# Performance work log

Hardware: AMD Instinct MI355X
Metric: run time of the kernel (lower is better)

The kernel has to match this reference:

```python
import jax, jax.numpy as jnp
import numpy as np

N = 10000
E = 160000
IN_C = 512
OUT_C = 1024
NEG_SLOPE = 0.2


def setup_inputs() -> dict:
    key = jax.random.key(0)
    ks = jax.random.split(key, 12)
    x = jax.random.normal(ks[0], (N, IN_C), dtype=jnp.float32)
    edge_index = jax.random.randint(ks[1], (2, E), 0, N, dtype=jnp.int32)
    s_in = 1.0 / np.sqrt(IN_C)
    s_out = 1.0 / np.sqrt(OUT_C)
    return {
        "x": x,
        "edge_index": edge_index,
        "W1": jax.random.normal(ks[2], (IN_C, OUT_C), dtype=jnp.float32) * s_in,
        "a_src1": jax.random.normal(ks[3], (OUT_C,), dtype=jnp.float32) * s_out,
        "a_dst1": jax.random.normal(ks[4], (OUT_C,), dtype=jnp.float32) * s_out,
        "b1": jnp.zeros((OUT_C,), dtype=jnp.float32),
        "W2": jax.random.normal(ks[5], (IN_C, OUT_C), dtype=jnp.float32) * s_in,
        "a_src2": jax.random.normal(ks[6], (OUT_C,), dtype=jnp.float32) * s_out,
        "a_dst2": jax.random.normal(ks[7], (OUT_C,), dtype=jnp.float32) * s_out,
        "b2": jnp.zeros((OUT_C,), dtype=jnp.float32),
        "prelu_a": jnp.asarray(0.25, dtype=jnp.float32),
        "Wp1": jax.random.normal(ks[8], (OUT_C, OUT_C), dtype=jnp.float32) * s_out,
        "bp1": jnp.zeros((OUT_C,), dtype=jnp.float32),
        "Wp2": jax.random.normal(ks[9], (OUT_C, 1024), dtype=jnp.float32) * s_out,
    }


def _gat_conv(x, src, dst, W, a_src, a_dst, b):
    # x: [N, in], W: [in, out]. PyG GATConv, heads=1, self-loops already in src/dst.
    h = x @ W  # [N, out]
    alpha_s = h @ a_src  # [N]
    alpha_d = h @ a_dst  # [N]
    e = alpha_s[src] + alpha_d[dst]  # [E+N]
    e = jnp.where(e >= 0, e, NEG_SLOPE * e)  # LeakyReLU(0.2)
    # segment softmax over destination nodes
    m = jax.ops.segment_max(e, dst, num_segments=N)  # [N]
    ex = jnp.exp(e - m[dst])
    denom = jax.ops.segment_sum(ex, dst, num_segments=N)  # [N], >=1 via self-loops
    alpha = ex / denom[dst]  # [E+N]
    out = jax.ops.segment_sum(alpha[:, None] * h[src], dst, num_segments=N)
    return out + b


def reference(x, edge_index, W1, a_src1, a_dst1, b1, W2, a_src2, a_dst2, b2,
              prelu_a, Wp1, bp1, Wp2):
    # add self loops (PyG GATConv default)
    loops = jnp.arange(N, dtype=edge_index.dtype)
    src = jnp.concatenate([edge_index[0], loops])
    dst = jnp.concatenate([edge_index[1], loops])

    def prelu(v):
        return jnp.where(v >= 0, v, prelu_a * v)

    h1 = prelu(_gat_conv(x, src, dst, W1, a_src1, a_dst1, b1))  # [N, 1024]
    h2 = prelu(_gat_conv(x, src, dst, W2, a_src2, a_dst2, b2))  # [N, 1024]
    h = h1 + h2

    # semantic attention: project -> mean over nodes -> softmax over 1024 dims
    w = jnp.tanh(h @ Wp1 + bp1) @ Wp2  # [N, 1024]
    w = w.mean(axis=0)  # [1024]
    att = jax.nn.softmax(w, axis=0)  # [1024] == beta.mean(0).squeeze()
    return att * h1 + (1.0 - att) * h2
```

## Files before the change

### kernel.cpp

```cpp
#include <hip/hip_runtime.h>

#define IN_C 512
#define OUT_C 1024
#define NC2 2048
#define NEG_SLOPE 0.2f

typedef short frag8 __attribute__((ext_vector_type(8)));
typedef float f32x4 __attribute__((ext_vector_type(4)));
typedef int i32x4 __attribute__((ext_vector_type(4)));

#define GLOAD_LDS16(g, l) __builtin_amdgcn_global_load_lds(\
    (const __attribute__((address_space(1))) void*)(g), \
    (__attribute__((address_space(3))) void*)(l), 16, 0, 0)

__device__ __forceinline__ unsigned short f2b(float f){
  unsigned u = __float_as_uint(f);
  unsigned r = (u + 0x7fffu + ((u >> 16) & 1u)) >> 16;
  return (unsigned short)r;
}
__device__ __forceinline__ unsigned encf(float f){
  unsigned u = __float_as_uint(f);
  return (u & 0x80000000u) ? ~u : (u | 0x80000000u);
}
__device__ __forceinline__ float decf(unsigned u){
  unsigned v = (u & 0x80000000u) ? (u & 0x7fffffffu) : ~u;
  return __uint_as_float(v);
}
__device__ __forceinline__ float leaky(float v){ return v >= 0.f ? v : NEG_SLOPE * v; }


__global__ void prep_kernel(const float* __restrict__ W1, const float* __restrict__ W2,
                            const float* __restrict__ Wp1,
                            const float* __restrict__ a_src1, const float* __restrict__ a_dst1,
                            const float* __restrict__ a_src2, const float* __restrict__ a_dst2,
                            unsigned short* __restrict__ WT, unsigned short* __restrict__ Wp1T,
                            float* __restrict__ uv){
  __shared__ float tile[32][33];
  int b = blockIdx.x;
  int tx = threadIdx.x & 31, ty = threadIdx.x >> 5;
  if (b < 1024){
    const float* in = (b >> 9) ? W2 : W1;
    int rowOff = (b >> 9) * OUT_C;
    int bb = b & 511;
    int c0 = (bb & 31) * 32, r0 = (bb >> 5) * 32;
    for (int i = ty; i < 32; i += 8)
      tile[i][tx] = in[(size_t)(r0 + i) * OUT_C + c0 + tx];
    __syncthreads();
    for (int i = ty; i < 32; i += 8)
      WT[(size_t)(c0 + i + rowOff) * IN_C + r0 + tx] = f2b(tile[tx][i]);
  } else if (b < 2048){
    int bb = b - 1024;
    int c0 = (bb & 31) * 32, r0 = (bb >> 5) * 32;
    for (int i = ty; i < 32; i += 8)
      tile[i][tx] = Wp1[(size_t)(r0 + i) * OUT_C + c0 + tx];
    __syncthreads();
    for (int i = ty; i < 32; i += 8)
      Wp1T[(size_t)(c0 + i) * OUT_C + r0 + tx] = f2b(tile[tx][i]);
  } else {
    int g = (b - 2048) * 4 + (threadIdx.x >> 6);
    int lane = threadIdx.x & 63;
    int which = g >> 9;
    int i = g & 511;
    const float* W = (which < 2) ? W1 : W2;
    const float* a = (which == 0) ? a_src1 : (which == 1) ? a_dst1 : (which == 2) ? a_src2 : a_dst2;
    const float* row = W + (size_t)i * OUT_C;
    float s = 0.f;
    for (int j = lane; j < OUT_C; j += 64) s += row[j] * a[j];
    for (int off = 32; off; off >>= 1) s += __shfl_down(s, off);
    if (lane == 0) uv[which * IN_C + i] = s;
  }
}


__global__ void alpha_kernel(const float* __restrict__ x, const float* __restrict__ uv,
                             unsigned short* __restrict__ xb,
                             float* __restrict__ as1, float* __restrict__ ad1,
                             float* __restrict__ as2, float* __restrict__ ad2,
                             float* __restrict__ self1, float* __restrict__ self2,
                             unsigned* __restrict__ m1e, unsigned* __restrict__ m2e,
                             int* counts, int* cursor, float* colsum, float* wv){
  int n = blockIdx.x;
  int w = threadIdx.x >> 6, lane = threadIdx.x & 63;
  __shared__ float sh[4];
  if (threadIdx.x == 0){ counts[n] = 0; cursor[n] = 0; }
  if (n < 8){
    int i = n * 256 + threadIdx.x;
    if (i < 1024) colsum[i] = 0.f; else wv[i - 1024] = 0.f;
  }
  const float* row = x + (size_t)n * IN_C;
  const float* u = uv + w * IN_C;
  float s = 0.f;
  for (int j = lane; j < IN_C; j += 64){
    float v = row[j];
    s += v * u[j];
    if (w == 0) xb[(size_t)n * IN_C + j] = f2b(v);
  }
  for (int off = 32; off; off >>= 1) s += __shfl_down(s, off);
  if (lane == 0){
    sh[w] = s;
    if (w == 0) as1[n] = s;
    else if (w == 1) ad1[n] = s;
    else if (w == 2) as2[n] = s;
    else ad2[n] = s;
  }
  __syncthreads();
  if (threadIdx.x == 0){
    float e1 = leaky(sh[0] + sh[1]);
    float e2 = leaky(sh[2] + sh[3]);
    self1[n] = e1; self2[n] = e2;
    m1e[n] = encf(e1); m2e[n] = encf(e2);
  }
}


__global__ void histmax_kernel(const int* __restrict__ src, const int* __restrict__ dst,
                               const float* __restrict__ as1, const float* __restrict__ ad1,
                               const float* __restrict__ as2, const float* __restrict__ ad2,
                               int* counts, unsigned* m1e, unsigned* m2e, int E){
  int e = blockIdx.x * 256 + threadIdx.x;
  if (e >= E) return;
  int s = src[e], d = dst[e];
  atomicAdd(&counts[d], 1);
  atomicMax(&m1e[d], encf(leaky(as1[s] + ad1[d])));
  atomicMax(&m2e[d], encf(leaky(as2[s] + ad2[d])));
}

__global__ void scanA_kernel(const int* __restrict__ counts, int* __restrict__ offs,
                             int* __restrict__ bsum, int n){
  __shared__ int wsum[4];
  int i = blockIdx.x * 256 + threadIdx.x;
  int wave = threadIdx.x >> 6, lane = threadIdx.x & 63;
  int v = (i < n) ? counts[i] : 0;
  int sc = v;
  for (int o = 1; o < 64; o <<= 1){
    int t = __shfl_up(sc, o);
    if (lane >= o) sc += t;
  }
  if (lane == 63) wsum[wave] = sc;
  __syncthreads();
  int wp = 0, tot = 0;
#pragma unroll
  for (int k = 0; k < 4; k++){
    int ws = wsum[k];
    if (k < wave) wp += ws;
    tot += ws;
  }
  if (i < n) offs[i] = wp + sc - v;
  if (threadIdx.x == 0) bsum[blockIdx.x] = tot;
}

__global__ void scanB_kernel(int* __restrict__ bsum, int nb){
  int lane = threadIdx.x;
  int v = (lane < nb) ? bsum[lane] : 0;
  int sc = v;
  for (int o = 1; o < 64; o <<= 1){
    int t = __shfl_up(sc, o);
    if (lane >= o) sc += t;
  }
  if (lane < nb) bsum[lane] = sc - v;
}

__global__ void scanC_kernel(int* __restrict__ offs, const int* __restrict__ bsum, int n){
  int i = blockIdx.x * 256 + threadIdx.x;
  if (i < n) offs[i] += bsum[blockIdx.x];
}

__global__ void denominit_kernel(const unsigned* __restrict__ m1e, const unsigned* __restrict__ m2e,
                                 const float* __restrict__ self1, const float* __restrict__ self2,
                                 float* __restrict__ m1, float* __restrict__ m2,
                                 float* __restrict__ den1, float* __restrict__ den2, int N){
  int i = blockIdx.x * 256 + threadIdx.x;
  if (i >= N) return;
  float a = decf(m1e[i]), b = decf(m2e[i]);
  m1[i] = a; m2[i] = b;
  den1[i] = expf(self1[i] - a);
  den2[i] = expf(self2[i] - b);
}

__global__ void scatterexp_kernel(const int* __restrict__ src, const int* __restrict__ dst,
                                  const int* __restrict__ offs, int* cursor,
                                  const float* __restrict__ as1, const float* __restrict__ ad1,
                                  const float* __restrict__ as2, const float* __restrict__ ad2,
                                  const float* __restrict__ m1, const float* __restrict__ m2,
                                  int* __restrict__ nsrc, float* __restrict__ nw1, float* __restrict__ nw2,
                                  float* den1, float* den2, int E){
  int e = blockIdx.x * 256 + threadIdx.x;
  if (e >= E) return;
  int s = src[e], d = dst[e];
  int p = atomicAdd(&cursor[d], 1);
  int idx = offs[d] + p;
  float x1 = expf(leaky(as1[s] + ad1[d]) - m1[d]);
  float x2 = expf(leaky(as2[s] + ad2[d]) - m2[d]);
  nsrc[idx] = s; nw1[idx] = x1; nw2[idx] = x2;
  atomicAdd(&den1[d], x1);
  atomicAdd(&den2[d], x2);
}


#define AGG_FMA8(ACC, W, U) \
  ACC[0] += (W) * __uint_as_float(((unsigned)(U).x) << 16); \
  ACC[1] += (W) * __uint_as_float(((unsigned)(U).x) & 0xffff0000u); \
  ACC[2] += (W) * __uint_as_float(((unsigned)(U).y) << 16); \
  ACC[3] += (W) * __uint_as_float(((unsigned)(U).y) & 0xffff0000u); \
  ACC[4] += (W) * __uint_as_float(((unsigned)(U).z) << 16); \
  ACC[5] += (W) * __uint_as_float(((unsigned)(U).z) & 0xffff0000u); \
  ACC[6] += (W) * __uint_as_float(((unsigned)(U).w) << 16); \
  ACC[7] += (W) * __uint_as_float(((unsigned)(U).w) & 0xffff0000u);

__global__ __launch_bounds__(256) void aggx_kernel(
    const int* __restrict__ counts, const int* __restrict__ offs,
    const int* __restrict__ nsrc, const float* __restrict__ nw1, const float* __restrict__ nw2,
    const float* __restrict__ den1, const float* __restrict__ den2,
    const float* __restrict__ self1, const float* __restrict__ self2,
    const float* __restrict__ m1, const float* __restrict__ m2,
    const unsigned short* __restrict__ xb,
    unsigned short* __restrict__ xa1b, unsigned short* __restrict__ xa2b, int N){
  int tid = threadIdx.x;
  int g = tid >> 4, hl = tid & 15;
  int grpbase = tid & 48;
  int d = blockIdx.y * 16 + g;
  if (d >= N) return;
  int colbase = blockIdx.x * 128 + hl * 8;
  float inv1 = 1.f / den1[d], inv2 = 1.f / den2[d];
  int deg = counts[d], off = offs[d];
  float acc1[8] = {0,0,0,0,0,0,0,0}, acc2[8] = {0,0,0,0,0,0,0,0};
  const unsigned short* Xb = xb + colbase;
  for (int base = 0; base < deg; base += 16){
    int i = base + hl;
    int s = 0; float w1 = 0.f, w2 = 0.f;
    if (i < deg){
      int p = off + i;
      s = nsrc[p];
      w1 = nw1[p] * inv1;
      w2 = nw2[p] * inv2;
    }
    int cnt = min(16, deg - base);
#pragma unroll 4
    for (int j = 0; j < cnt; j++){
      int sj = __shfl(s, grpbase + j);
      float w1j = __shfl(w1, grpbase + j);
      float w2j = __shfl(w2, grpbase + j);
      int4 u = *(const int4*)(Xb + (size_t)sj * IN_C);
      AGG_FMA8(acc1, w1j, u)
      AGG_FMA8(acc2, w2j, u)
    }
  }
  {
    float ws1 = expf(self1[d] - m1[d]) * inv1;
    float ws2 = expf(self2[d] - m2[d]) * inv2;
    int4 u = *(const int4*)(Xb + (size_t)d * IN_C);
    AGG_FMA8(acc1, ws1, u)
    AGG_FMA8(acc2, ws2, u)
  }
  size_t outb = (size_t)d * IN_C + colbase;
  i32x4 o1, o2;
  o1.x = (int)((unsigned)f2b(acc1[0]) | ((unsigned)f2b(acc1[1]) << 16));
  o1.y = (int)((unsigned)f2b(acc1[2]) | ((unsigned)f2b(acc1[3]) << 16));
  o1.z = (int)((unsigned)f2b(acc1[4]) | ((unsigned)f2b(acc1[5]) << 16));
  o1.w = (int)((unsigned)f2b(acc1[6]) | ((unsigned)f2b(acc1[7]) << 16));
  o2.x = (int)((unsigned)f2b(acc2[0]) | ((unsigned)f2b(acc2[1]) << 16));
  o2.y = (int)((unsigned)f2b(acc2[2]) | ((unsigned)f2b(acc2[3]) << 16));
  o2.z = (int)((unsigned)f2b(acc2[4]) | ((unsigned)f2b(acc2[5]) << 16));
  o2.w = (int)((unsigned)f2b(acc2[6]) | ((unsigned)f2b(acc2[7]) << 16));
  __builtin_nontemporal_store(o1, (i32x4*)(xa1b + outb));
  __builtin_nontemporal_store(o2, (i32x4*)(xa2b + outb));
}


__global__ __launch_bounds__(256, 2) void gemmh_kernel(const unsigned short* __restrict__ A1,
                                                       const unsigned short* __restrict__ A2,
                                                       const unsigned short* __restrict__ BT,
                                                       const float* __restrict__ b1,
                                                       const float* __restrict__ b2,
                                                       const float* __restrict__ prelu_a,
                                                       unsigned short* __restrict__ hsum,
                                                       unsigned short* __restrict__ hdiff,
                                                       int M, int Mtiles, int perx){
  const int bid = blockIdx.x;
  const int xcd = bid & 7;
  const int li = bid >> 3;
  const int bn_t = li & 7;
  const int bm_t = xcd * perx + (li >> 3);
  if (bm_t >= Mtiles) return;
  const int bm = bm_t * 128, bn = bn_t * 128;
  __shared__ unsigned short Al[2][128 * 32];
  __shared__ unsigned short Bl[2][128 * 32];
  const int t = threadIdx.x;
  const int lane = t & 63, wid = t >> 6;
  const int wr = wid >> 1, wc = wid & 1;
  const int l16 = lane & 15, q = lane >> 4;
  const int qs = (q ^ ((l16 >> 1) & 3)) * 8;
  const int lch = (((lane & 3) ^ ((lane >> 3) & 3)) * 8);
  f32x4 acc1[4][4] = {};
  f32x4 acc2[4][4] = {};
  const int srow = wid * 32 + (lane >> 2);
  const int ga0 = min(bm + srow, M - 1);
  const int ga1 = min(bm + srow + 16, M - 1);
  const unsigned short* pa1_0 = A1 + (size_t)ga0 * IN_C + lch;
  const unsigned short* pa1_1 = A1 + (size_t)ga1 * IN_C + lch;
  const unsigned short* pa2_0 = A2 + (size_t)ga0 * IN_C + lch;
  const unsigned short* pa2_1 = A2 + (size_t)ga1 * IN_C + lch;
  const unsigned short* pb1_0 = BT + (size_t)(bn + srow) * IN_C + lch;
  const unsigned short* pb1_1 = BT + (size_t)(bn + srow + 16) * IN_C + lch;
  const unsigned short* pb2_0 = pb1_0 + (size_t)OUT_C * IN_C;
  const unsigned short* pb2_1 = pb1_1 + (size_t)OUT_C * IN_C;
  const int so0 = (wid * 32) * 32;
  const int so1 = (wid * 32 + 16) * 32;

  for (int k0 = 0; k0 < IN_C; k0 += 32){
    GLOAD_LDS16(pa1_0 + k0, &Al[0][so0]);
    GLOAD_LDS16(pa1_1 + k0, &Al[0][so1]);
    GLOAD_LDS16(pa2_0 + k0, &Al[1][so0]);
    GLOAD_LDS16(pa2_1 + k0, &Al[1][so1]);
    GLOAD_LDS16(pb1_0 + k0, &Bl[0][so0]);
    GLOAD_LDS16(pb1_1 + k0, &Bl[0][so1]);
    GLOAD_LDS16(pb2_0 + k0, &Bl[1][so0]);
    GLOAD_LDS16(pb2_1 + k0, &Bl[1][so1]);
    __syncthreads();
    {
      frag8 af[4], bf[4];
#pragma unroll
      for (int mi = 0; mi < 4; mi++) af[mi] = *(const frag8*)&Al[0][(wr*64 + mi*16 + l16) * 32 + qs];
#pragma unroll
      for (int nj = 0; nj < 4; nj++) bf[nj] = *(const frag8*)&Bl[0][(wc*64 + nj*16 + l16) * 32 + qs];
#pragma unroll
      for (int mi = 0; mi < 4; mi++)
#pragma unroll
        for (int nj = 0; nj < 4; nj++)
          acc1[mi][nj] = __builtin_amdgcn_mfma_f32_16x16x32_bf16(af[mi], bf[nj], acc1[mi][nj], 0, 0, 0);
    }
    {
      frag8 af[4], bf[4];
#pragma unroll
      for (int mi = 0; mi < 4; mi++) af[mi] = *(const frag8*)&Al[1][(wr*64 + mi*16 + l16) * 32 + qs];
#pragma unroll
      for (int nj = 0; nj < 4; nj++) bf[nj] = *(const frag8*)&Bl[1][(wc*64 + nj*16 + l16) * 32 + qs];
#pragma unroll
      for (int mi = 0; mi < 4; mi++)
#pragma unroll
        for (int nj = 0; nj < 4; nj++)
          acc2[mi][nj] = __builtin_amdgcn_mfma_f32_16x16x32_bf16(af[mi], bf[nj], acc2[mi][nj], 0, 0, 0);
    }
    __syncthreads();
  }

  float pa = prelu_a[0];
#pragma unroll
  for (int mi = 0; mi < 4; mi++){
#pragma unroll
    for (int r = 0; r < 4; r++){
      int row = bm + wr*64 + mi*16 + q*4 + r;
      if (row >= M) continue;
#pragma unroll
      for (int nj = 0; nj < 4; nj++){
        int col = bn + wc*64 + nj*16 + l16;
        float v1 = acc1[mi][nj][r] + b1[col];
        v1 = v1 >= 0.f ? v1 : pa * v1;
        float v2 = acc2[mi][nj][r] + b2[col];
        v2 = v2 >= 0.f ? v2 : pa * v2;
        size_t idx = (size_t)row * OUT_C + col;
        __builtin_nontemporal_store(f2b(v1 + v2), &hsum[idx]);
        __builtin_nontemporal_store(f2b(v1 - v2), &hdiff[idx]);
      }
    }
  }
}


__global__ __launch_bounds__(256, 2) void gemm2_kernel(const unsigned short* __restrict__ A,
                                                       const unsigned short* __restrict__ BT,
                                                       const float* __restrict__ bp1,
                                                       float* __restrict__ colsum,
                                                       int M, int Mtiles, int perx){
  const int bid = blockIdx.x;
  const int xcd = bid & 7;
  const int li = bid >> 3;
  const int bn_t = li & 7;
  const int bm_t = xcd * perx + (li >> 3);
  if (bm_t >= Mtiles) return;
  const int bm = bm_t * 128, bn = bn_t * 128;
  __shared__ unsigned short Al[128 * 32];
  __shared__ unsigned short Bl[128 * 32];
  __shared__ float cs[128];
  const int t = threadIdx.x;
  const int lane = t & 63, wid = t >> 6;
  const int wr = wid >> 1, wc = wid & 1;
  const int l16 = lane & 15, q = lane >> 4;
  const int qs = (q ^ ((l16 >> 1) & 3)) * 8;
  const int lch = (((lane & 3) ^ ((lane >> 3) & 3)) * 8);
  if (t < 128) cs[t] = 0.f;
  f32x4 acc[4][4] = {};
  const int srow = wid * 32 + (lane >> 2);
  const int ga0 = min(bm + srow, M - 1);
  const int ga1 = min(bm + srow + 16, M - 1);
  const unsigned short* pa_0 = A + (size_t)ga0 * OUT_C + lch;
  const unsigned short* pa_1 = A + (size_t)ga1 * OUT_C + lch;
  const unsigned short* pb_0 = BT + (size_t)(bn + srow) * OUT_C + lch;
  const unsigned short* pb_1 = BT + (size_t)(bn + srow + 16) * OUT_C + lch;
  const int so0 = (wid * 32) * 32;
  const int so1 = (wid * 32 + 16) * 32;

  for (int k0 = 0; k0 < OUT_C; k0 += 32){
    GLOAD_LDS16(pa_0 + k0, &Al[so0]);
    GLOAD_LDS16(pa_1 + k0, &Al[so1]);
    GLOAD_LDS16(pb_0 + k0, &Bl[so0]);
    GLOAD_LDS16(pb_1 + k0, &Bl[so1]);
    __syncthreads();
    frag8 af[4], bf[4];
#pragma unroll
    for (int mi = 0; mi < 4; mi++) af[mi] = *(const frag8*)&Al[(wr*64 + mi*16 + l16) * 32 + qs];
#pragma unroll
    for (int nj = 0; nj < 4; nj++) bf[nj] = *(const frag8*)&Bl[(wc*64 + nj*16 + l16) * 32 + qs];
#pragma unroll
    for (int mi = 0; mi < 4; mi++)
#pragma unroll
      for (int nj = 0; nj < 4; nj++)
        acc[mi][nj] = __builtin_amdgcn_mfma_f32_16x16x32_bf16(af[mi], bf[nj], acc[mi][nj], 0, 0, 0);
    __syncthreads();
  }

#pragma unroll
  for (int nj = 0; nj < 4; nj++){
    int col = bn + wc*64 + nj*16 + l16;
    float bias = bp1[col];
    float p = 0.f;
#pragma unroll
    for (int mi = 0; mi < 4; mi++){
#pragma unroll
      for (int r = 0; r < 4; r++){
        int row = bm + wr*64 + mi*16 + q*4 + r;
        float tv = tanhf(acc[mi][nj][r] + bias);
        if (row < M) p += tv;
      }
    }
    p += __shfl_xor(p, 16);
    p += __shfl_xor(p, 32);
    if (q == 0) atomicAdd(&cs[wc*64 + nj*16 + l16], p);
  }
  __syncthreads();
  if (t < 128) atomicAdd(&colsum[bn + t], cs[t]);
}


__global__ void wproj_kernel(const float* __restrict__ colsum, const float* __restrict__ Wp2,
                             float* __restrict__ wv){
  int o = blockIdx.x * 256 + threadIdx.x;
  int c0 = blockIdx.y * 128;
  float acc = 0.f;
  for (int c = c0; c < c0 + 128; c++) acc += colsum[c] * Wp2[(size_t)c * OUT_C + o];
  atomicAdd(&wv[o], acc);
}

__global__ __launch_bounds__(1024) void softmax_kernel(const float* __restrict__ wv,
                                                       float* __restrict__ att, float invN){
  int o = threadIdx.x;
  __shared__ float red[1024];
  float w = wv[o] * invN;
  red[o] = w; __syncthreads();
  for (int s = 512; s > 0; s >>= 1){ if (o < s) red[o] = fmaxf(red[o], red[o + s]); __syncthreads(); }
  float m = red[0]; __syncthreads();
  float e = expf(w - m);
  red[o] = e; __syncthreads();
  for (int s = 512; s > 0; s >>= 1){ if (o < s) red[o] += red[o + s]; __syncthreads(); }
  att[o] = e / red[0];
}

__global__ void combine_kernel(const float* __restrict__ att, const unsigned short* __restrict__ hs,
                               const unsigned short* __restrict__ hd, float* __restrict__ out, int total8){
  int i = blockIdx.x * 256 + threadIdx.x;
  if (i >= total8) return;
  int colb = (i & 127) * 8;
  int4 us = ((const int4*)hs)[i];
  int4 ud = ((const int4*)hd)[i];
  float4 a0 = *(const float4*)(att + colb);
  float4 a1 = *(const float4*)(att + colb + 4);
  float o[8]; float sv, dv;
  sv = __uint_as_float(((unsigned)us.x) << 16);        dv = __uint_as_float(((unsigned)ud.x) << 16);
  o[0] = 0.5f * sv + (a0.x - 0.5f) * dv;
  sv = __uint_as_float(((unsigned)us.x) & 0xffff0000u); dv = __uint_as_float(((unsigned)ud.x) & 0xffff0000u);
  o[1] = 0.5f * sv + (a0.y - 0.5f) * dv;
  sv = __uint_as_float(((unsigned)us.y) << 16);        dv = __uint_as_float(((unsigned)ud.y) << 16);
  o[2] = 0.5f * sv + (a0.z - 0.5f) * dv;
  sv = __uint_as_float(((unsigned)us.y) & 0xffff0000u); dv = __uint_as_float(((unsigned)ud.y) & 0xffff0000u);
  o[3] = 0.5f * sv + (a0.w - 0.5f) * dv;
  sv = __uint_as_float(((unsigned)us.z) << 16);        dv = __uint_as_float(((unsigned)ud.z) << 16);
  o[4] = 0.5f * sv + (a1.x - 0.5f) * dv;
  sv = __uint_as_float(((unsigned)us.z) & 0xffff0000u); dv = __uint_as_float(((unsigned)ud.z) & 0xffff0000u);
  o[5] = 0.5f * sv + (a1.y - 0.5f) * dv;
  sv = __uint_as_float(((unsigned)us.w) << 16);        dv = __uint_as_float(((unsigned)ud.w) << 16);
  o[6] = 0.5f * sv + (a1.z - 0.5f) * dv;
  sv = __uint_as_float(((unsigned)us.w) & 0xffff0000u); dv = __uint_as_float(((unsigned)ud.w) & 0xffff0000u);
  o[7] = 0.5f * sv + (a1.w - 0.5f) * dv;
  f32x4 f0; f0[0] = o[0]; f0[1] = o[1]; f0[2] = o[2]; f0[3] = o[3];
  f32x4 f1; f1[0] = o[4]; f1[1] = o[5]; f1[2] = o[6]; f1[3] = o[7];
  __builtin_nontemporal_store(f0, (f32x4*)(out + (size_t)i * 8));
  __builtin_nontemporal_store(f1, (f32x4*)(out + (size_t)i * 8 + 4));
}


extern "C" void kernel_launch(void* const* d_in, const int* in_sizes, int n_in,
                              void* d_out, int out_size, void* d_ws, size_t ws_size,
                              hipStream_t stream){
  const float* x      = (const float*)d_in[0];
  const int*   edge   = (const int*)d_in[1];
  const float* W1     = (const float*)d_in[2];
  const float* a_src1 = (const float*)d_in[3];
  const float* a_dst1 = (const float*)d_in[4];
  const float* b1     = (const float*)d_in[5];
  const float* W2     = (const float*)d_in[6];
  const float* a_src2 = (const float*)d_in[7];
  const float* a_dst2 = (const float*)d_in[8];
  const float* b2     = (const float*)d_in[9];
  const float* prelu_a= (const float*)d_in[10];
  const float* Wp1    = (const float*)d_in[11];
  const float* bp1    = (const float*)d_in[12];
  const float* Wp2    = (const float*)d_in[13];
  const int N = in_sizes[0] / IN_C;
  const int E = in_sizes[1] / 2;
  const int* srcArr = edge;
  const int* dstArr = edge + E;

  char* ws = (char*)d_ws;
  size_t o = 0;
  auto alloc = [&](size_t b) -> char* {
    char* p = ws + o;
    o = (o + b + 255) & ~(size_t)255;
    return p;
  };
  unsigned short* xb    = (unsigned short*)alloc((size_t)N * IN_C * 2);
  unsigned short* WT    = (unsigned short*)alloc((size_t)NC2 * IN_C * 2);
  unsigned short* Wp1T  = (unsigned short*)alloc((size_t)OUT_C * OUT_C * 2);
  unsigned short* xa1b  = (unsigned short*)alloc((size_t)N * IN_C * 2);
  unsigned short* xa2b  = (unsigned short*)alloc((size_t)N * IN_C * 2);
  unsigned short* hsum  = (unsigned short*)alloc((size_t)N * OUT_C * 2);
  unsigned short* hdiff = (unsigned short*)alloc((size_t)N * OUT_C * 2);
  float*          uv    = (float*)alloc(4 * IN_C * 4);
  float*          as1   = (float*)alloc((size_t)4 * N * 4);
  float* ad1 = as1 + N; float* as2 = as1 + 2 * N; float* ad2 = as1 + 3 * N;
  float*          self1 = (float*)alloc((size_t)2 * N * 4); float* self2 = self1 + N;
  unsigned*       m1e   = (unsigned*)alloc((size_t)2 * N * 4); unsigned* m2e = m1e + N;
  float*          m1    = (float*)alloc((size_t)2 * N * 4); float* m2 = m1 + N;
  float*          den1  = (float*)alloc((size_t)2 * N * 4); float* den2 = den1 + N;
  int*            counts= (int*)alloc((size_t)N * 4);
  int*            offs  = (int*)alloc((size_t)(N + 1) * 4);
  int*            cursor= (int*)alloc((size_t)N * 4);
  int*            bsum  = (int*)alloc(64 * 4);
  int*            nsrc  = (int*)alloc((size_t)E * 4);
  float*          nw1   = (float*)alloc((size_t)E * 4);
  float*          nw2   = (float*)alloc((size_t)E * 4);
  float*          colsum= (float*)alloc(OUT_C * 4);
  float*          wv    = (float*)alloc(OUT_C * 4);
  float*          att   = (float*)alloc(OUT_C * 4);

  const int Mtiles = (N + 127) / 128;
  const int perx = (Mtiles + 7) / 8;
  const int gemmgrid = 8 * perx * 8;
  const int nchunk = (N + 255) / 256;

  prep_kernel<<<2560, 256, 0, stream>>>(W1, W2, Wp1, a_src1, a_dst1, a_src2, a_dst2, WT, Wp1T, uv);
  alpha_kernel<<<N, 256, 0, stream>>>(x, uv, xb, as1, ad1, as2, ad2, self1, self2, m1e, m2e,
                                      counts, cursor, colsum, wv);
  histmax_kernel<<<(E + 255) / 256, 256, 0, stream>>>(srcArr, dstArr, as1, ad1, as2, ad2,
                                                      counts, m1e, m2e, E);
  scanA_kernel<<<nchunk, 256, 0, stream>>>(counts, offs, bsum, N);
  scanB_kernel<<<1, 64, 0, stream>>>(bsum, nchunk);
  scanC_kernel<<<nchunk, 256, 0, stream>>>(offs, bsum, N);
  denominit_kernel<<<nchunk, 256, 0, stream>>>(m1e, m2e, self1, self2, m1, m2, den1, den2, N);
  scatterexp_kernel<<<(E + 255) / 256, 256, 0, stream>>>(srcArr, dstArr, offs, cursor,
                                                         as1, ad1, as2, ad2, m1, m2,
                                                         nsrc, nw1, nw2, den1, den2, E);
  aggx_kernel<<<dim3(4, (N + 15) / 16), 256, 0, stream>>>(counts, offs, nsrc, nw1, nw2, den1, den2,
                                                          self1, self2, m1, m2, xb, xa1b, xa2b, N);
  gemmh_kernel<<<gemmgrid, 256, 0, stream>>>(xa1b, xa2b, WT, b1, b2, prelu_a,
                                             hsum, hdiff, N, Mtiles, perx);
  gemm2_kernel<<<gemmgrid, 256, 0, stream>>>(hsum, Wp1T, bp1, colsum, N, Mtiles, perx);
  wproj_kernel<<<dim3(4, 8), 256, 0, stream>>>(colsum, Wp2, wv);
  softmax_kernel<<<1, 1024, 0, stream>>>(wv, att, 1.0f / (float)N);
  combine_kernel<<<(N * OUT_C / 8 + 255) / 256, 256, 0, stream>>>(att, hsum, hdiff, (float*)d_out,
                                                                  N * OUT_C / 8);
}
```

Baseline: 339.3 us.

## Use 256x256 triple-buffered GEMM tiles and store h1/h2 instead of sum/diff

Both GEMMs move from 128x128 tiles with 256 threads to 256x256 tiles with 512 threads and a three-stage LDS pipeline that waits with explicit vmcnt counts, so each step needs one barrier instead of two. gemmh now computes h1 and h2 in separate blocks and stores them directly. gemm2 forms h1+h2 on the fly by loading both through registers and adding them in bf16 before writing to LDS. The aim is more data reuse per block and better overlap of loads with MFMA work. The cost is heavier register and LDS pressure, an extra global read stream in gemm2, and a different tile-to-XCD mapping.

```diff
diff --git a/kernel.cpp b/kernel.cpp
--- a/kernel.cpp
+++ b/kernel.cpp
@@ -27,6 +27,13 @@
   return __uint_as_float(v);
 }
 __device__ __forceinline__ float leaky(float v){ return v >= 0.f ? v : NEG_SLOPE * v; }
+__device__ __forceinline__ int badd(int a, int b){
+  float a0 = __uint_as_float(((unsigned)a) << 16);
+  float a1 = __uint_as_float(((unsigned)a) & 0xffff0000u);
+  float b0 = __uint_as_float(((unsigned)b) << 16);
+  float b1 = __uint_as_float(((unsigned)b) & 0xffff0000u);
+  return (int)((unsigned)f2b(a0 + b0) | ((unsigned)f2b(a1 + b1) << 16));
+}
 
 
 __global__ void prep_kernel(const float* __restrict__ W1, const float* __restrict__ W2,
@@ -267,157 +274,178 @@
 }
 
 
-__global__ __launch_bounds__(256, 2) void gemmh_kernel(const unsigned short* __restrict__ A1,
+#define COMP256(AB, BB) do{ \
+    frag8 af[8], bf[4]; \
+    _Pragma("unroll") \
+    for (int mi = 0; mi < 8; mi++) af[mi] = *(const frag8*)&(AB)[(wr*128 + mi*16 + l16) * 32 + qs]; \
+    _Pragma("unroll") \
+    for (int nj = 0; nj < 4; nj++) bf[nj] = *(const frag8*)&(BB)[(wc*64 + nj*16 + l16) * 32 + qs]; \
+    _Pragma("unroll") \
+    for (int mi = 0; mi < 8; mi++) \
+      _Pragma("unroll") \
+      for (int nj = 0; nj < 4; nj++) \
+        acc[mi][nj] = __builtin_amdgcn_mfma_f32_16x16x32_bf16(af[mi], bf[nj], acc[mi][nj], 0, 0, 0); \
+  }while(0)
+
+
+__global__ __launch_bounds__(512, 2) void gemmh_kernel(const unsigned short* __restrict__ A1,
                                                        const unsigned short* __restrict__ A2,
                                                        const unsigned short* __restrict__ BT,
                                                        const float* __restrict__ b1,
                                                        const float* __restrict__ b2,
                                                        const float* __restrict__ prelu_a,
-                                                       unsigned short* __restrict__ hsum,
-                                                       unsigned short* __restrict__ hdiff,
-                                                       int M, int Mtiles, int perx){
-  const int bid = blockIdx.x;
-  const int xcd = bid & 7;
-  const int li = bid >> 3;
-  const int bn_t = li & 7;
-  const int bm_t = xcd * perx + (li >> 3);
-  if (bm_t >= Mtiles) return;
-  const int bm = bm_t * 128, bn = bn_t * 128;
-  __shared__ unsigned short Al[2][128 * 32];
-  __shared__ unsigned short Bl[2][128 * 32];
+                                                       unsigned short* __restrict__ h1,
+                                                       unsigned short* __restrict__ h2,
+                                                       int M, int Mtiles){
+  const int per = Mtiles;
+  const int sw = (blockIdx.x & 7) * per + (blockIdx.x >> 3);
+  const int bm = (sw >> 3) * 256;
+  const int g  = (sw >> 2) & 1;
+  const int bn = (sw & 3) * 256;
+  __shared__ unsigned short Al[3][256 * 32];
+  __shared__ unsigned short Bl[3][256 * 32];
   const int t = threadIdx.x;
   const int lane = t & 63, wid = t >> 6;
-  const int wr = wid >> 1, wc = wid & 1;
+  const int wr = wid >> 2, wc = wid & 3;
   const int l16 = lane & 15, q = lane >> 4;
   const int qs = (q ^ ((l16 >> 1) & 3)) * 8;
   const int lch = (((lane & 3) ^ ((lane >> 3) & 3)) * 8);
-  f32x4 acc1[4][4] = {};
-  f32x4 acc2[4][4] = {};
-  const int srow = wid * 32 + (lane >> 2);
-  const int ga0 = min(bm + srow, M - 1);
-  const int ga1 = min(bm + srow + 16, M - 1);
-  const unsigned short* pa1_0 = A1 + (size_t)ga0 * IN_C + lch;
-  const unsigned short* pa1_1 = A1 + (size_t)ga1 * IN_C + lch;
-  const unsigned short* pa2_0 = A2 + (size_t)ga0 * IN_C + lch;
-  const unsigned short* pa2_1 = A2 + (size_t)ga1 * IN_C + lch;
-  const unsigned short* pb1_0 = BT + (size_t)(bn + srow) * IN_C + lch;
-  const unsigned short* pb1_1 = BT + (size_t)(bn + srow + 16) * IN_C + lch;
-  const unsigned short* pb2_0 = pb1_0 + (size_t)OUT_C * IN_C;
-  const unsigned short* pb2_1 = pb1_1 + (size_t)OUT_C * IN_C;
-  const int so0 = (wid * 32) * 32;
-  const int so1 = (wid * 32 + 16) * 32;
-
-  for (int k0 = 0; k0 < IN_C; k0 += 32){
-    GLOAD_LDS16(pa1_0 + k0, &Al[0][so0]);
-    GLOAD_LDS16(pa1_1 + k0, &Al[0][so1]);
-    GLOAD_LDS16(pa2_0 + k0, &Al[1][so0]);
-    GLOAD_LDS16(pa2_1 + k0, &Al[1][so1]);
-    GLOAD_LDS16(pb1_0 + k0, &Bl[0][so0]);
-    GLOAD_LDS16(pb1_1 + k0, &Bl[0][so1]);
-    GLOAD_LDS16(pb2_0 + k0, &Bl[1][so0]);
-    GLOAD_LDS16(pb2_1 + k0, &Bl[1][so1]);
-    __syncthreads();
-    {
-      frag8 af[4], bf[4];
-#pragma unroll
-      for (int mi = 0; mi < 4; mi++) af[mi] = *(const frag8*)&Al[0][(wr*64 + mi*16 + l16) * 32 + qs];
-#pragma unroll
-      for (int nj = 0; nj < 4; nj++) bf[nj] = *(const frag8*)&Bl[0][(wc*64 + nj*16 + l16) * 32 + qs];
-#pragma unroll
-      for (int mi = 0; mi < 4; mi++)
-#pragma unroll
-        for (int nj = 0; nj < 4; nj++)
-          acc1[mi][nj] = __builtin_amdgcn_mfma_f32_16x16x32_bf16(af[mi], bf[nj], acc1[mi][nj], 0, 0, 0);
-    }
-    {
-      frag8 af[4], bf[4];
-#pragma unroll
-      for (int mi = 0; mi < 4; mi++) af[mi] = *(const frag8*)&Al[1][(wr*64 + mi*16 + l16) * 32 + qs];
-#pragma unroll
-      for (int nj = 0; nj < 4; nj++) bf[nj] = *(const frag8*)&Bl[1][(wc*64 + nj*16 + l16) * 32 + qs];
-#pragma unroll
-      for (int mi = 0; mi < 4; mi++)
-#pragma unroll
-        for (int nj = 0; nj < 4; nj++)
-          acc2[mi][nj] = __builtin_amdgcn_mfma_f32_16x16x32_bf16(af[mi], bf[nj], acc2[mi][nj], 0, 0, 0);
-    }
-    __syncthreads();
-  }
-
+  f32x4 acc[8][4] = {};
+  const unsigned short* Asrc = g ? A2 : A1;
+  const int r0 = wid * 16 + (lane >> 2);
+  const unsigned short* pa0 = Asrc + (size_t)min(bm + r0,       M - 1) * IN_C + lch;
+  const unsigned short* pa1 = Asrc + (size_t)min(bm + r0 + 128, M - 1) * IN_C + lch;
+  const unsigned short* pb0 = BT + (size_t)(g * OUT_C + bn + r0      ) * IN_C + lch;
+  const unsigned short* pb1 = BT + (size_t)(g * OUT_C + bn + r0 + 128) * IN_C + lch;
+  const int so0 = (wid * 16) * 32;
+  const int so1 = (wid * 16 + 128) * 32;
+
+#define STGH(B, k0) do{ \
+    GLOAD_LDS16(pa0 + (k0), &Al[B][so0]); \
+    GLOAD_LDS16(pa1 + (k0), &Al[B][so1]); \
+    GLOAD_LDS16(pb0 + (k0), &Bl[B][so0]); \
+    GLOAD_LDS16(pb1 + (k0), &Bl[B][so1]); \
+  }while(0)
+
+  STGH(0, 0);
+  STGH(1, 32);
+  int cur = 0;
+#pragma unroll 1
+  for (int it = 0; it < 16; ++it){
+    asm volatile("s_waitcnt vmcnt(4)" ::: "memory");
+    __builtin_amdgcn_s_barrier();
+    int nb = cur ? cur - 1 : 2;
+    int kc = it + 2 > 15 ? 15 : it + 2;
+    STGH(nb, kc * 32);
+    COMP256(Al[cur], Bl[cur]);
+    cur = cur < 2 ? cur + 1 : 0;
+  }
+#undef STGH
+
+  const float* bias = g ? b2 : b1;
+  unsigned short* H = g ? h2 : h1;
   float pa = prelu_a[0];
 #pragma unroll
-  for (int mi = 0; mi < 4; mi++){
+  for (int mi = 0; mi < 8; mi++){
 #pragma unroll
     for (int r = 0; r < 4; r++){
-      int row = bm + wr*64 + mi*16 + q*4 + r;
+      int row = bm + wr*128 + mi*16 + q*4 + r;
       if (row >= M) continue;
 #pragma unroll
       for (int nj = 0; nj < 4; nj++){
         int col = bn + wc*64 + nj*16 + l16;
-        float v1 = acc1[mi][nj][r] + b1[col];
-        v1 = v1 >= 0.f ? v1 : pa * v1;
-        float v2 = acc2[mi][nj][r] + b2[col];
-        v2 = v2 >= 0.f ? v2 : pa * v2;
-        size_t idx = (size_t)row * OUT_C + col;
-        __builtin_nontemporal_store(f2b(v1 + v2), &hsum[idx]);
-        __builtin_nontemporal_store(f2b(v1 - v2), &hdiff[idx]);
+        float v = acc[mi][nj][r] + bias[col];
+        v = v >= 0.f ? v : pa * v;
+        __builtin_nontemporal_store(f2b(v), &H[(size_t)row * OUT_C + col]);
       }
     }
   }
 }
 
 
-__global__ __launch_bounds__(256, 2) void gemm2_kernel(const unsigned short* __restrict__ A,
+__global__ __launch_bounds__(512, 2) void gemm2_kernel(const unsigned short* __restrict__ h1,
+                                                       const unsigned short* __restrict__ h2,
                                                        const unsigned short* __restrict__ BT,
                                                        const float* __restrict__ bp1,
                                                        float* __restrict__ colsum,
-                                                       int M, int Mtiles, int perx){
+                                                       int M, int Mtiles){
+  const int nwg = Mtiles * 4;
   const int bid = blockIdx.x;
-  const int xcd = bid & 7;
-  const int li = bid >> 3;
-  const int bn_t = li & 7;
-  const int bm_t = xcd * perx + (li >> 3);
-  if (bm_t >= Mtiles) return;
-  const int bm = bm_t * 128, bn = bn_t * 128;
-  __shared__ unsigned short Al[128 * 32];
-  __shared__ unsigned short Bl[128 * 32];
-  __shared__ float cs[128];
+  const int sw = (nwg & 7) ? bid : ((bid & 7) * (nwg >> 3) + (bid >> 3));
+  const int bm = (sw >> 2) * 256;
+  const int bn = (sw & 3) * 256;
+  __shared__ unsigned short Al[3][256 * 32];
+  __shared__ unsigned short Bl[3][256 * 32];
+  __shared__ float cs[256];
   const int t = threadIdx.x;
   const int lane = t & 63, wid = t >> 6;
-  const int wr = wid >> 1, wc = wid & 1;
+  const int wr = wid >> 2, wc = wid & 3;
   const int l16 = lane & 15, q = lane >> 4;
   const int qs = (q ^ ((l16 >> 1) & 3)) * 8;
   const int lch = (((lane & 3) ^ ((lane >> 3) & 3)) * 8);
-  if (t < 128) cs[t] = 0.f;
-  f32x4 acc[4][4] = {};
-  const int srow = wid * 32 + (lane >> 2);
-  const int ga0 = min(bm + srow, M - 1);
-  const int ga1 = min(bm + srow + 16, M - 1);
-  const unsigned short* pa_0 = A + (size_t)ga0 * OUT_C + lch;
-  const unsigned short* pa_1 = A + (size_t)ga1 * OUT_C + lch;
-  const unsigned short* pb_0 = BT + (size_t)(bn + srow) * OUT_C + lch;
-  const unsigned short* pb_1 = BT + (size_t)(bn + srow + 16) * OUT_C + lch;
-  const int so0 = (wid * 32) * 32;
-  const int so1 = (wid * 32 + 16) * 32;
-
-  for (int k0 = 0; k0 < OUT_C; k0 += 32){
-    GLOAD_LDS16(pa_0 + k0, &Al[so0]);
-    GLOAD_LDS16(pa_1 + k0, &Al[so1]);
-    GLOAD_LDS16(pb_0 + k0, &Bl[so0]);
-    GLOAD_LDS16(pb_1 + k0, &Bl[so1]);
-    __syncthreads();
-    frag8 af[4], bf[4];
-#pragma unroll
-    for (int mi = 0; mi < 4; mi++) af[mi] = *(const frag8*)&Al[(wr*64 + mi*16 + l16) * 32 + qs];
-#pragma unroll
-    for (int nj = 0; nj < 4; nj++) bf[nj] = *(const frag8*)&Bl[(wc*64 + nj*16 + l16) * 32 + qs];
-#pragma unroll
-    for (int mi = 0; mi < 4; mi++)
-#pragma unroll
-      for (int nj = 0; nj < 4; nj++)
-        acc[mi][nj] = __builtin_amdgcn_mfma_f32_16x16x32_bf16(af[mi], bf[nj], acc[mi][nj], 0, 0, 0);
-    __syncthreads();
-  }
+  if (t < 256) cs[t] = 0.f;
+  f32x4 acc[8][4] = {};
+  const int r0 = wid * 16 + (lane >> 2);
+  const unsigned short* pb0 = BT + (size_t)(bn + r0      ) * OUT_C + lch;
+  const unsigned short* pb1 = BT + (size_t)(bn + r0 + 128) * OUT_C + lch;
+  const int so0 = (wid * 16) * 32;
+  const int so1 = (wid * 16 + 128) * 32;
+  const int ra = t >> 1, hc = t & 1;
+  const size_t arowoff = (size_t)min(bm + ra, M - 1) * OUT_C + hc * 16;
+  const unsigned short* ph1 = h1 + arowoff;
+  const unsigned short* ph2 = h2 + arowoff;
+  const int rs = (ra >> 1) & 3;
+  const int wa0 = ra * 32 + ((hc * 2) ^ rs) * 8;
+  const int wa1 = ra * 32 + ((hc * 2 + 1) ^ rs) * 8;
+  int4 pA_h1a, pA_h1b, pA_h2a, pA_h2b;
+  int4 pB_h1a, pB_h1b, pB_h2a, pB_h2b;
+
+#define LOADA(D1A, D1B, D2A, D2B, KC) do{ \
+    D1A = *(const int4*)(ph1 + (KC) * 32); \
+    D1B = *(const int4*)(ph1 + (KC) * 32 + 8); \
+    D2A = *(const int4*)(ph2 + (KC) * 32); \
+    D2B = *(const int4*)(ph2 + (KC) * 32 + 8); \
+  }while(0)
+#define WRITEA(NW, C1A, C1B, C2A, C2B) do{ \
+    int4 w0, w1; \
+    w0.x = badd((C1A).x, (C2A).x); w0.y = badd((C1A).y, (C2A).y); \
+    w0.z = badd((C1A).z, (C2A).z); w0.w = badd((C1A).w, (C2A).w); \
+    w1.x = badd((C1B).x, (C2B).x); w1.y = badd((C1B).y, (C2B).y); \
+    w1.z = badd((C1B).z, (C2B).z); w1.w = badd((C1B).w, (C2B).w); \
+    *(int4*)&Al[NW][wa0] = w0; \
+    *(int4*)&Al[NW][wa1] = w1; \
+  }while(0)
+#define G2BODY(T, C1A, C1B, C2A, C2B, N1A, N1B, N2A, N2B) do{ \
+    asm volatile("s_waitcnt vmcnt(2)" ::: "memory"); \
+    asm volatile("s_waitcnt lgkmcnt(0)" ::: "memory"); \
+    __builtin_amdgcn_s_barrier(); \
+    int kc = (T) + 2 > 31 ? 31 : (T) + 2; \
+    LOADA(N1A, N1B, N2A, N2B, kc); \
+    GLOAD_LDS16(pb0 + kc * 32, &Bl[nb][so0]); \
+    GLOAD_LDS16(pb1 + kc * 32, &Bl[nb][so1]); \
+    WRITEA(nw, C1A, C1B, C2A, C2B); \
+    COMP256(Al[cur], Bl[cur]); \
+    cur = cur < 2 ? cur + 1 : 0; \
+    nb  = nb  < 2 ? nb  + 1 : 0; \
+    nw  = nw  < 2 ? nw  + 1 : 0; \
+  }while(0)
+
+  LOADA(pA_h1a, pA_h1b, pA_h2a, pA_h2b, 0);
+  GLOAD_LDS16(pb0, &Bl[0][so0]);
+  GLOAD_LDS16(pb1, &Bl[0][so1]);
+  LOADA(pB_h1a, pB_h1b, pB_h2a, pB_h2b, 1);
+  GLOAD_LDS16(pb0 + 32, &Bl[1][so0]);
+  GLOAD_LDS16(pb1 + 32, &Bl[1][so1]);
+  WRITEA(0, pA_h1a, pA_h1b, pA_h2a, pA_h2b);
+  int cur = 0, nb = 2, nw = 1;
+#pragma unroll 1
+  for (int it = 0; it < 32; it += 2){
+    G2BODY(it,     pB_h1a, pB_h1b, pB_h2a, pB_h2b, pA_h1a, pA_h1b, pA_h2a, pA_h2b);
+    G2BODY(it + 1, pA_h1a, pA_h1b, pA_h2a, pA_h2b, pB_h1a, pB_h1b, pB_h2a, pB_h2b);
+  }
+#undef G2BODY
+#undef WRITEA
+#undef LOADA
 
 #pragma unroll
   for (int nj = 0; nj < 4; nj++){
@@ -425,10 +453,10 @@
     float bias = bp1[col];
     float p = 0.f;
 #pragma unroll
-    for (int mi = 0; mi < 4; mi++){
+    for (int mi = 0; mi < 8; mi++){
 #pragma unroll
       for (int r = 0; r < 4; r++){
-        int row = bm + wr*64 + mi*16 + q*4 + r;
+        int row = bm + wr*128 + mi*16 + q*4 + r;
         float tv = tanhf(acc[mi][nj][r] + bias);
         if (row < M) p += tv;
       }
@@ -438,7 +466,7 @@
     if (q == 0) atomicAdd(&cs[wc*64 + nj*16 + l16], p);
   }
   __syncthreads();
-  if (t < 128) atomicAdd(&colsum[bn + t], cs[t]);
+  if (t < 256) atomicAdd(&colsum[bn + t], cs[t]);
 }
 
 
@@ -465,32 +493,32 @@
   att[o] = e / red[0];
 }
 
-__global__ void combine_kernel(const float* __restrict__ att, const unsigned short* __restrict__ hs,
-                               const unsigned short* __restrict__ hd, float* __restrict__ out, int total8){
+__global__ void combine_kernel(const float* __restrict__ att, const unsigned short* __restrict__ h1,
+                               const unsigned short* __restrict__ h2, float* __restrict__ out, int total8){
   int i = blockIdx.x * 256 + threadIdx.x;
   if (i >= total8) return;
   int colb = (i & 127) * 8;
-  int4 us = ((const int4*)hs)[i];
-  int4 ud = ((const int4*)hd)[i];
+  int4 u1 = ((const int4*)h1)[i];
+  int4 u2 = ((const int4*)h2)[i];
   float4 a0 = *(const float4*)(att + colb);
   float4 a1 = *(const float4*)(att + colb + 4);
-  float o[8]; float sv, dv;
-  sv = __uint_as_float(((unsigned)us.x) << 16);        dv = __uint_as_float(((unsigned)ud.x) << 16);
-  o[0] = 0.5f * sv + (a0.x - 0.5f) * dv;
-  sv = __uint_as_float(((unsigned)us.x) & 0xffff0000u); dv = __uint_as_float(((unsigned)ud.x) & 0xffff0000u);
-  o[1] = 0.5f * sv + (a0.y - 0.5f) * dv;
-  sv = __uint_as_float(((unsigned)us.y) << 16);        dv = __uint_as_float(((unsigned)ud.y) << 16);
-  o[2] = 0.5f * sv + (a0.z - 0.5f) * dv;
-  sv = __uint_as_float(((unsigned)us.y) & 0xffff0000u); dv = __uint_as_float(((unsigned)ud.y) & 0xffff0000u);
-  o[3] = 0.5f * sv + (a0.w - 0.5f) * dv;
-  sv = __uint_as_float(((unsigned)us.z) << 16);        dv = __uint_as_float(((unsigned)ud.z) << 16);
-  o[4] = 0.5f * sv + (a1.x - 0.5f) * dv;
-  sv = __uint_as_float(((unsigned)us.z) & 0xffff0000u); dv = __uint_as_float(((unsigned)ud.z) & 0xffff0000u);
-  o[5] = 0.5f * sv + (a1.y - 0.5f) * dv;
-  sv = __uint_as_float(((unsigned)us.w) << 16);        dv = __uint_as_float(((unsigned)ud.w) << 16);
-  o[6] = 0.5f * sv + (a1.z - 0.5f) * dv;
-  sv = __uint_as_float(((unsigned)us.w) & 0xffff0000u); dv = __uint_as_float(((unsigned)ud.w) & 0xffff0000u);
-  o[7] = 0.5f * sv + (a1.w - 0.5f) * dv;
+  float o[8]; float v1, v2;
+  v1 = __uint_as_float(((unsigned)u1.x) << 16);         v2 = __uint_as_float(((unsigned)u2.x) << 16);
+  o[0] = v2 + a0.x * (v1 - v2);
+  v1 = __uint_as_float(((unsigned)u1.x) & 0xffff0000u); v2 = __uint_as_float(((unsigned)u2.x) & 0xffff0000u);
+  o[1] = v2 + a0.y * (v1 - v2);
+  v1 = __uint_as_float(((unsigned)u1.y) << 16);         v2 = __uint_as_float(((unsigned)u2.y) << 16);
+  o[2] = v2 + a0.z * (v1 - v2);
+  v1 = __uint_as_float(((unsigned)u1.y) & 0xffff0000u); v2 = __uint_as_float(((unsigned)u2.y) & 0xffff0000u);
+  o[3] = v2 + a0.w * (v1 - v2);
+  v1 = __uint_as_float(((unsigned)u1.z) << 16);         v2 = __uint_as_float(((unsigned)u2.z) << 16);
+  o[4] = v2 + a1.x * (v1 - v2);
+  v1 = __uint_as_float(((unsigned)u1.z) & 0xffff0000u); v2 = __uint_as_float(((unsigned)u2.z) & 0xffff0000u);
+  o[5] = v2 + a1.y * (v1 - v2);
+  v1 = __uint_as_float(((unsigned)u1.w) << 16);         v2 = __uint_as_float(((unsigned)u2.w) << 16);
+  o[6] = v2 + a1.z * (v1 - v2);
+  v1 = __uint_as_float(((unsigned)u1.w) & 0xffff0000u); v2 = __uint_as_float(((unsigned)u2.w) & 0xffff0000u);
+  o[7] = v2 + a1.w * (v1 - v2);
   f32x4 f0; f0[0] = o[0]; f0[1] = o[1]; f0[2] = o[2]; f0[3] = o[3];
   f32x4 f1; f1[0] = o[4]; f1[1] = o[5]; f1[2] = o[6]; f1[3] = o[7];
   __builtin_nontemporal_store(f0, (f32x4*)(out + (size_t)i * 8));
@@ -532,8 +560,8 @@
   unsigned short* Wp1T  = (unsigned short*)alloc((size_t)OUT_C * OUT_C * 2);
   unsigned short* xa1b  = (unsigned short*)alloc((size_t)N * IN_C * 2);
   unsigned short* xa2b  = (unsigned short*)alloc((size_t)N * IN_C * 2);
-  unsigned short* hsum  = (unsigned short*)alloc((size_t)N * OUT_C * 2);
-  unsigned short* hdiff = (unsigned short*)alloc((size_t)N * OUT_C * 2);
+  unsigned short* h1    = (unsigned short*)alloc((size_t)N * OUT_C * 2);
+  unsigned short* h2    = (unsigned short*)alloc((size_t)N * OUT_C * 2);
   float*          uv    = (float*)alloc(4 * IN_C * 4);
   float*          as1   = (float*)alloc((size_t)4 * N * 4);
   float* ad1 = as1 + N; float* as2 = as1 + 2 * N; float* ad2 = as1 + 3 * N;
@@ -552,9 +580,7 @@
   float*          wv    = (float*)alloc(OUT_C * 4);
   float*          att   = (float*)alloc(OUT_C * 4);
 
-  const int Mtiles = (N + 127) / 128;
-  const int perx = (Mtiles + 7) / 8;
-  const int gemmgrid = 8 * perx * 8;
+  const int Mt = (N + 255) / 256;
   const int nchunk = (N + 255) / 256;
 
   prep_kernel<<<2560, 256, 0, stream>>>(W1, W2, Wp1, a_src1, a_dst1, a_src2, a_dst2, WT, Wp1T, uv);
@@ -571,11 +597,10 @@
                                                          nsrc, nw1, nw2, den1, den2, E);
   aggx_kernel<<<dim3(4, (N + 15) / 16), 256, 0, stream>>>(counts, offs, nsrc, nw1, nw2, den1, den2,
                                                           self1, self2, m1, m2, xb, xa1b, xa2b, N);
-  gemmh_kernel<<<gemmgrid, 256, 0, stream>>>(xa1b, xa2b, WT, b1, b2, prelu_a,
-                                             hsum, hdiff, N, Mtiles, perx);
-  gemm2_kernel<<<gemmgrid, 256, 0, stream>>>(hsum, Wp1T, bp1, colsum, N, Mtiles, perx);
+  gemmh_kernel<<<Mt * 8, 512, 0, stream>>>(xa1b, xa2b, WT, b1, b2, prelu_a, h1, h2, N, Mt);
+  gemm2_kernel<<<Mt * 4, 512, 0, stream>>>(h1, h2, Wp1T, bp1, colsum, N, Mt);
   wproj_kernel<<<dim3(4, 8), 256, 0, stream>>>(colsum, Wp2, wv);
   softmax_kernel<<<1, 1024, 0, stream>>>(wv, att, 1.0f / (float)N);
-  combine_kernel<<<(N * OUT_C / 8 + 255) / 256, 256, 0, stream>>>(att, hsum, hdiff, (float*)d_out,
+  combine_kernel<<<(N * OUT_C / 8 + 255) / 256, 256, 0, stream>>>(att, h1, h2, (float*)d_out,
                                                                   N * OUT_C / 8);
 }
```

Result: slower. 387.6 us (+14.2%).
